# Kernel tuning notes

Measured on AMD Instinct MI355X. Metric: run time of the kernel, lower is better.

## Reference

```python
import jax, jax.numpy as jnp
import numpy as np


def setup_inputs() -> dict:
    key = jax.random.key(0)
    k1, k2, k3 = jax.random.split(key, 3)
    bs, seqlen, hidden = 2, 2048, 1024
    s, h = 4, 256  # sqrt_n_heads, head_size
    std = 0.02
    num_layers = 12
    hidden_states = jax.random.normal(k1, (bs, seqlen, hidden), dtype=jnp.float32)
    q_scale = 1.0 / np.sqrt(2.0 * num_layers * h)
    queries = jax.random.normal(k2, (s, h, h * s), dtype=jnp.float32) * std * q_scale
    combiners = jax.random.normal(k3, (s, h * s, h), dtype=jnp.float32) * (std * q_scale)
    return {"hidden_states": hidden_states, "queries": queries, "combiners": combiners}


def reference(hidden_states, queries, combiners):
    # queries: [s1, h, s*h], combiners: [s1, s*h, h]
    s, h, _ = queries.shape
    bs, S, E = hidden_states.shape
    x = hidden_states.reshape(bs, S, s, h)            # [b, t, s, h]
    qw = queries.reshape(s, h, s, h)                  # [s1, h_in, s2, h_out]
    # projected queries, already permuted to [s2, b, t, s1, f]
    Q = jnp.einsum('btae,aeqf->qbtaf', x, qw)
    # pre-attention scores: [s2, b, t, s1, u] (u = key position)  ~O(S^2)
    pre = jnp.einsum('qbtaf,buqf->qbtau', Q, x)
    # attention output, permuted to [s1, b, t, s2, g]
    attn = jnp.einsum('qbtau,buqg->abtqg', pre, x)
    attn = attn.reshape(s, bs, S, s * h)              # [s1, b, t, s2*h]
    out = jnp.einsum('abtk,akg->btag', attn, combiners)
    return out.reshape(bs, S, s * h)
```

## Files before the change

### kernel.cpp

```cpp
#include <hip/hip_runtime.h>
#include <hip/hip_bf16.h>


typedef unsigned short u16;
using short8  = __attribute__((ext_vector_type(8))) short;
using floatx4 = __attribute__((ext_vector_type(4))) float;

__device__ inline u16 f2bf(float f) {
    unsigned u = __float_as_uint(f);
    unsigned r = u + 0x7fffu + ((u >> 16) & 1u);
    return (u16)(r >> 16);
}

template <typename T>
__device__ inline void stage64(const T* __restrict__ src, long ld,
                               u16* __restrict__ dst, int tid) {
#pragma unroll
    for (int it = 0; it < 4; ++it) {
        const int flat = (it * 256 + tid) * 4;
        const int kl = flat & 63, rl = flat >> 6;
        ushort4 v;
        if (sizeof(T) == 4) {
            const float4 f = *(const float4*)&((const float*)src)[(long)rl * ld + kl];
            v.x = f2bf(f.x); v.y = f2bf(f.y); v.z = f2bf(f.z); v.w = f2bf(f.w);
        } else {
            v = *(const ushort4*)&((const u16*)src)[(long)rl * ld + kl];
        }
        const int chunk = ((kl >> 5) * 4 + (rl >> 4)) * 64 + ((kl >> 3) & 3) * 16 + (rl & 15);
        *(ushort4*)&dst[chunk * 8 + (kl & 7)] = v;
    }
}

__device__ inline void stage64_sum8(const float* __restrict__ s0, long ld,
                                    long partStride,
                                    u16* __restrict__ dst, int tid) {
#pragma unroll
    for (int it = 0; it < 4; ++it) {
        const int flat = (it * 256 + tid) * 4;
        const int kl = flat & 63, rl = flat >> 6;
        const long off = (long)rl * ld + kl;
        float4 acc = *(const float4*)&s0[off];
#pragma unroll
        for (int s = 1; s < 8; ++s) {
            const float4 f = *(const float4*)&s0[(long)s * partStride + off];
            acc.x += f.x; acc.y += f.y; acc.z += f.z; acc.w += f.w;
        }
        ushort4 v;
        v.x = f2bf(acc.x); v.y = f2bf(acc.y); v.z = f2bf(acc.z); v.w = f2bf(acc.w);
        const int chunk = ((kl >> 5) * 4 + (rl >> 4)) * 64 + ((kl >> 3) & 3) * 16 + (rl & 15);
        *(ushort4*)&dst[chunk * 8 + (kl & 7)] = v;
    }
}

__device__ inline void stage_km64(const float* __restrict__ src, long ld,
                                  u16* __restrict__ dst, int tid) {
#pragma unroll
    for (int it = 0; it < 4; ++it) {
        const int flat = (it * 256 + tid) * 4;
        const int m = flat & 63, k = flat >> 6;
        const float4 f = *(const float4*)&src[(long)k * ld + m];
        const int cb_ = ((k >> 5) * 4 + (m >> 4)) * 64 + ((k & 31) >> 3) * 16 + (m & 15);
        const int j = k & 7;
        dst[(cb_ + 0) * 8 + j] = f2bf(f.x);
        dst[(cb_ + 1) * 8 + j] = f2bf(f.y);
        dst[(cb_ + 2) * 8 + j] = f2bf(f.z);
        dst[(cb_ + 3) * 8 + j] = f2bf(f.w);
    }
}

template <typename TA, typename TB, typename TC,
          bool AKM, bool BKM, bool BSUM8, bool ATOMIC>
__device__ inline void gemm_tile(const TA* __restrict__ A, long lda,
                                 const TB* __restrict__ B, long ldb,
                                 long partStride,
                                 TC* __restrict__ C, long ldc,
                                 int m0, int n0) {
    __shared__ u16 As[16384];
    __shared__ u16 Bs[16384];
    const int tid = threadIdx.x, lane = tid & 63, w = tid >> 6;
    const int IA = (w & 1) * 2, JB = (w >> 1) * 2;
    floatx4 acc[2][2] = {};

#pragma unroll
    for (int kb = 0; kb < 4; ++kb) {
        if (AKM) stage_km64((const float*)A + (long)(kb * 64) * lda, lda, As + kb * 4096, tid);
        else     stage64(A + kb * 64, lda, As + kb * 4096, tid);
    }
#pragma unroll
    for (int kb = 0; kb < 4; ++kb) {
        if (BSUM8)    stage64_sum8((const float*)B + kb * 64, ldb, partStride, Bs + kb * 4096, tid);
        else if (BKM) stage_km64((const float*)B + (long)(kb * 64) * ldb, ldb, Bs + kb * 4096, tid);
        else          stage64(B + kb * 64, ldb, Bs + kb * 4096, tid);
    }
    __syncthreads();

#pragma unroll
    for (int kb = 0; kb < 4; ++kb)
#pragma unroll
        for (int s = 0; s < 2; ++s) {
            short8 af[2], bfr[2];
#pragma unroll
            for (int i = 0; i < 2; ++i)
                af[i] = *(const short8*)&As[kb * 4096 + ((s * 4 + IA + i) * 64 + lane) * 8];
#pragma unroll
            for (int j = 0; j < 2; ++j)
                bfr[j] = *(const short8*)&Bs[kb * 4096 + ((s * 4 + JB + j) * 64 + lane) * 8];
#pragma unroll
            for (int i = 0; i < 2; ++i)
#pragma unroll
                for (int j = 0; j < 2; ++j)
                    acc[i][j] = __builtin_amdgcn_mfma_f32_16x16x32_bf16(af[i], bfr[j], acc[i][j], 0, 0, 0);
        }

    const int rb = (lane >> 4) * 4, col = lane & 15;
#pragma unroll
    for (int i = 0; i < 2; ++i)
#pragma unroll
        for (int j = 0; j < 2; ++j)
#pragma unroll
            for (int r = 0; r < 4; ++r) {
                const int gm = m0 + (IA + i) * 16 + rb + r;
                const int gn = n0 + (JB + j) * 16 + col;
                TC* p = &C[(long)gm * ldc + gn];
                if (sizeof(TC) == 2) *(u16*)p = f2bf(acc[i][j][r]);
                else if (ATOMIC) atomicAdd((float*)p, acc[i][j][r]);
                else *(float*)p = acc[i][j][r];
            }
}

__device__ inline void stage_km128(const float* __restrict__ src, long ld,
                                   u16* __restrict__ dst, int tid) {
#pragma unroll
    for (int it = 0; it < 8; ++it) {
        const int flat = (it * 256 + tid) * 4;
        const int m = flat & 127, k = flat >> 7;
        const float4 f = *(const float4*)&src[(long)k * ld + m];
        const int cb_ = ((k >> 5) * 8 + (m >> 4)) * 64 + ((k & 31) >> 3) * 16 + (m & 15);
        const int j = k & 7;
        dst[(cb_ + 0) * 8 + j] = f2bf(f.x);
        dst[(cb_ + 1) * 8 + j] = f2bf(f.y);
        dst[(cb_ + 2) * 8 + j] = f2bf(f.z);
        dst[(cb_ + 3) * 8 + j] = f2bf(f.w);
    }
}

__global__ __launch_bounds__(256) void k_gram(const float* __restrict__ x,
                                              float* __restrict__ Gp,
                                              float* __restrict__ Wt) {
    __shared__ u16 As[16384];
    __shared__ u16 Bs[16384];
    const int tl = blockIdx.x, bq = blockIdx.y, split = blockIdx.z;
    const int tm = tl >> 1, tn = tl & 1;
    const int b = bq >> 2, q = bq & 3;
    const int tid = threadIdx.x, lane = tid & 63, w = tid >> 6;
    const int IA2 = (w & 1), JB2 = (w >> 1);

    {
        const int bl = tl + 4 * bq + 32 * split;
        float4 zero = {0.f, 0.f, 0.f, 0.f};
        float4* wz = (float4*)(Wt + (long)bl * 2048) + tid;
        wz[0] = zero; wz[256] = zero;
    }

    const float* base = x + (long)b * 2097152 + (long)split * 256 * 1024 + q * 256;
    const float* A = base + tm * 128;
    const float* B = base + tn * 128;
    floatx4 acc[4][4] = {};

#pragma unroll
    for (int burst = 0; burst < 2; ++burst) {
        if (burst) __syncthreads();
#pragma unroll
        for (int kb = 0; kb < 2; ++kb) {
            const long kk = burst * 128 + kb * 64;
            stage_km128(A + kk * 1024, 1024, As + kb * 8192, tid);
            stage_km128(B + kk * 1024, 1024, Bs + kb * 8192, tid);
        }
        __syncthreads();
#pragma unroll
        for (int kb = 0; kb < 2; ++kb)
#pragma unroll
            for (int s = 0; s < 2; ++s) {
                short8 af[4], bfr[4];
#pragma unroll
                for (int i = 0; i < 4; ++i)
                    af[i] = *(const short8*)&As[kb * 8192 + ((s * 8 + IA2 * 4 + i) * 64 + lane) * 8];
#pragma unroll
                for (int j = 0; j < 4; ++j)
                    bfr[j] = *(const short8*)&Bs[kb * 8192 + ((s * 8 + JB2 * 4 + j) * 64 + lane) * 8];
#pragma unroll
                for (int i = 0; i < 4; ++i)
#pragma unroll
                    for (int j = 0; j < 4; ++j)
                        acc[i][j] = __builtin_amdgcn_mfma_f32_16x16x32_bf16(af[i], bfr[j], acc[i][j], 0, 0, 0);
            }
    }

    float* C = Gp + (long)(split * 8 + bq) * 65536;
    const int rb = (lane >> 4) * 4, col = lane & 15;
#pragma unroll
    for (int i = 0; i < 4; ++i)
#pragma unroll
        for (int j = 0; j < 4; ++j)
#pragma unroll
            for (int r = 0; r < 4; ++r) {
                const int gm = tm * 128 + IA2 * 64 + i * 16 + rb + r;
                const int gn = tn * 128 + JB2 * 64 + j * 16 + col;
                C[(long)gm * 256 + gn] = acc[i][j][r];
            }
}

__global__ __launch_bounds__(256) void k_2a(const float* __restrict__ comb,
                                            const float* __restrict__ Gp,
                                            u16* __restrict__ Tt) {
    const int tile = blockIdx.x, i = blockIdx.y;
    const int tm = tile >> 2, tn = tile & 3;
    const int q = i & 3, ba = i >> 2, b = ba >> 2, a = ba & 3;
    gemm_tile<float, float, u16, true, false, true, false>(
        comb + (long)a * 262144 + (long)q * 256 * 256 + tm * 64, 256,
        Gp + (long)(b * 4 + q) * 65536 + (long)tn * 64 * 256, 256,
        (long)8 * 65536,
        Tt + (long)ba * 262144, 1024,
        tm * 64, q * 256 + tn * 64);
}

__global__ __launch_bounds__(256) void k_2b(const u16* __restrict__ Tt,
                                            const float* __restrict__ qw,
                                            float* __restrict__ Wt) {
    const int tile = blockIdx.x, ba = blockIdx.y, split = blockIdx.z;
    const int tm = tile >> 2, tn = tile & 3;
    const int a = ba & 3;
    gemm_tile<u16, float, float, false, false, false, true>(
        Tt + (long)ba * 262144 + (long)tm * 64 * 1024 + split * 256, 1024,
        qw + (long)a * 262144 + (long)tn * 64 * 1024 + split * 256, 1024, 0,
        Wt + (long)ba * 65536, 256,
        tm * 64, tn * 64);
}

__global__ __launch_bounds__(256) void k_3(const float* __restrict__ x,
                                           const float* __restrict__ Wt,
                                           float* __restrict__ out) {
    const int tl = blockIdx.x, ba = blockIdx.y;
    const int tm = tl >> 2, tn = tl & 3;
    const int b = ba >> 2, a = ba & 3;
    gemm_tile<float, float, float, false, false, false, false>(
        x + (long)b * 2097152 + (long)tm * 64 * 1024 + a * 256, 1024,
        Wt + (long)ba * 65536 + (long)tn * 64 * 256, 256, 0,
        out + (long)b * 2097152 + a * 256, 1024,
        tm * 64, tn * 64);
}

extern "C" void kernel_launch(void* const* d_in, const int* in_sizes, int n_in,
                              void* d_out, int out_size, void* d_ws, size_t ws_size,
                              hipStream_t stream) {
    const float* x    = (const float*)d_in[0];
    const float* qw   = (const float*)d_in[1];
    const float* comb = (const float*)d_in[2];
    float* out = (float*)d_out;

    char* ws = (char*)d_ws;
    float* Gp = (float*)(ws);
    float* Wt = (float*)(ws + (16u << 20));
    u16*   Tt = (u16*)  (ws + (18u << 20));

    k_gram<<<dim3(4, 8, 8),  256, 0, stream>>>(x, Gp, Wt);
    k_2a  <<<dim3(16, 32),   256, 0, stream>>>(comb, Gp, Tt);
    k_2b  <<<dim3(16, 8, 4), 256, 0, stream>>>(Tt, qw, Wt);
    k_3   <<<dim3(128, 8),   256, 0, stream>>>(x, Wt, out);
}
```

Before: 137.6 us.

## Pre-convert input to bf16 once and add separate split-K reduction kernel

Adds a kernel that converts hidden_states to bf16 once, so the Gram and final GEMM kernels read half-size bf16 data instead of converting fp32 at every staging. Adds a separate reduction kernel that sums the eight split-K Gram partials into one buffer, so k_2a no longer sums partials while loading its operands. This trades two extra launches and extra workspace traffic for less redundant conversion and less load work in the downstream GEMMs.

```diff
diff --git a/kernel.cpp b/kernel.cpp
--- a/kernel.cpp
+++ b/kernel.cpp
@@ -128,23 +128,46 @@
             }
 }
 
-__device__ inline void stage_km128(const float* __restrict__ src, long ld,
-                                   u16* __restrict__ dst, int tid) {
-#pragma unroll
-    for (int it = 0; it < 8; ++it) {
-        const int flat = (it * 256 + tid) * 4;
+__global__ __launch_bounds__(256) void k_cvt(const float* __restrict__ x,
+                                             u16* __restrict__ xbf) {
+    const long i = ((long)blockIdx.x * 256 + threadIdx.x) * 8;
+    const float4 a = *(const float4*)&x[i];
+    const float4 b = *(const float4*)&x[i + 4];
+    ushort4 lo, hi;
+    lo.x = f2bf(a.x); lo.y = f2bf(a.y); lo.z = f2bf(a.z); lo.w = f2bf(a.w);
+    hi.x = f2bf(b.x); hi.y = f2bf(b.y); hi.z = f2bf(b.z); hi.w = f2bf(b.w);
+    *(ushort4*)&xbf[i]     = lo;
+    *(ushort4*)&xbf[i + 4] = hi;
+}
+
+__global__ __launch_bounds__(256) void k_gred(const float* __restrict__ Gp,
+                                              float* __restrict__ Gs) {
+    const long i = ((long)blockIdx.x * 256 + threadIdx.x) * 4;
+    float4 acc = *(const float4*)&Gp[i];
+#pragma unroll
+    for (int s = 1; s < 8; ++s) {
+        const float4 f = *(const float4*)&Gp[(long)s * 524288 + i];
+        acc.x += f.x; acc.y += f.y; acc.z += f.z; acc.w += f.w;
+    }
+    *(float4*)&Gs[i] = acc;
+}
+
+__device__ inline void stage_km128_bf(const u16* __restrict__ src, long ld,
+                                      u16* __restrict__ dst, int tid) {
+#pragma unroll
+    for (int it = 0; it < 4; ++it) {
+        const int flat = (it * 256 + tid) * 8;
         const int m = flat & 127, k = flat >> 7;
-        const float4 f = *(const float4*)&src[(long)k * ld + m];
+        const short8 v = *(const short8*)&src[(long)k * ld + m];
         const int cb_ = ((k >> 5) * 8 + (m >> 4)) * 64 + ((k & 31) >> 3) * 16 + (m & 15);
         const int j = k & 7;
-        dst[(cb_ + 0) * 8 + j] = f2bf(f.x);
-        dst[(cb_ + 1) * 8 + j] = f2bf(f.y);
-        dst[(cb_ + 2) * 8 + j] = f2bf(f.z);
-        dst[(cb_ + 3) * 8 + j] = f2bf(f.w);
-    }
-}
-
-__global__ __launch_bounds__(256) void k_gram(const float* __restrict__ x,
+#pragma unroll
+        for (int e = 0; e < 8; ++e)
+            dst[(cb_ + e) * 8 + j] = (u16)v[e];
+    }
+}
+
+__global__ __launch_bounds__(256) void k_gram(const u16* __restrict__ xbf,
                                               float* __restrict__ Gp,
                                               float* __restrict__ Wt) {
     __shared__ u16 As[16384];
@@ -162,9 +185,9 @@
         wz[0] = zero; wz[256] = zero;
     }
 
-    const float* base = x + (long)b * 2097152 + (long)split * 256 * 1024 + q * 256;
-    const float* A = base + tm * 128;
-    const float* B = base + tn * 128;
+    const u16* base = xbf + (long)b * 2097152 + (long)split * 256 * 1024 + q * 256;
+    const u16* A = base + tm * 128;
+    const u16* B = base + tn * 128;
     floatx4 acc[4][4] = {};
 
 #pragma unroll
@@ -173,8 +196,8 @@
 #pragma unroll
         for (int kb = 0; kb < 2; ++kb) {
             const long kk = burst * 128 + kb * 64;
-            stage_km128(A + kk * 1024, 1024, As + kb * 8192, tid);
-            stage_km128(B + kk * 1024, 1024, Bs + kb * 8192, tid);
+            stage_km128_bf(A + kk * 1024, 1024, As + kb * 8192, tid);
+            stage_km128_bf(B + kk * 1024, 1024, Bs + kb * 8192, tid);
         }
         __syncthreads();
 #pragma unroll
@@ -211,15 +234,15 @@
 }
 
 __global__ __launch_bounds__(256) void k_2a(const float* __restrict__ comb,
-                                            const float* __restrict__ Gp,
+                                            const float* __restrict__ Gs,
                                             u16* __restrict__ Tt) {
     const int tile = blockIdx.x, i = blockIdx.y;
     const int tm = tile >> 2, tn = tile & 3;
     const int q = i & 3, ba = i >> 2, b = ba >> 2, a = ba & 3;
-    gemm_tile<float, float, u16, true, false, true, false>(
+    gemm_tile<float, float, u16, true, false, false, false>(
         comb + (long)a * 262144 + (long)q * 256 * 256 + tm * 64, 256,
-        Gp + (long)(b * 4 + q) * 65536 + (long)tn * 64 * 256, 256,
-        (long)8 * 65536,
+        Gs + (long)(b * 4 + q) * 65536 + (long)tn * 64 * 256, 256,
+        0,
         Tt + (long)ba * 262144, 1024,
         tm * 64, q * 256 + tn * 64);
 }
@@ -237,14 +260,14 @@
         tm * 64, tn * 64);
 }
 
-__global__ __launch_bounds__(256) void k_3(const float* __restrict__ x,
+__global__ __launch_bounds__(256) void k_3(const u16* __restrict__ xbf,
                                            const float* __restrict__ Wt,
                                            float* __restrict__ out) {
     const int tl = blockIdx.x, ba = blockIdx.y;
     const int tm = tl >> 2, tn = tl & 3;
     const int b = ba >> 2, a = ba & 3;
-    gemm_tile<float, float, float, false, false, false, false>(
-        x + (long)b * 2097152 + (long)tm * 64 * 1024 + a * 256, 1024,
+    gemm_tile<u16, float, float, false, false, false, false>(
+        xbf + (long)b * 2097152 + (long)tm * 64 * 1024 + a * 256, 1024,
         Wt + (long)ba * 65536 + (long)tn * 64 * 256, 256, 0,
         out + (long)b * 2097152 + a * 256, 1024,
         tm * 64, tn * 64);
@@ -262,9 +285,13 @@
     float* Gp = (float*)(ws);
     float* Wt = (float*)(ws + (16u << 20));
     u16*   Tt = (u16*)  (ws + (18u << 20));
-
-    k_gram<<<dim3(4, 8, 8),  256, 0, stream>>>(x, Gp, Wt);
-    k_2a  <<<dim3(16, 32),   256, 0, stream>>>(comb, Gp, Tt);
+    float* Gs = (float*)(ws + (22u << 20));
+    u16*   xbf= (u16*)  (ws + (24u << 20));
+
+    k_cvt <<<dim3(2048),     256, 0, stream>>>(x, xbf);
+    k_gram<<<dim3(4, 8, 8),  256, 0, stream>>>(xbf, Gp, Wt);
+    k_gred<<<dim3(512),      256, 0, stream>>>(Gp, Gs);
+    k_2a  <<<dim3(16, 32),   256, 0, stream>>>(comb, Gs, Tt);
     k_2b  <<<dim3(16, 8, 4), 256, 0, stream>>>(Tt, qw, Wt);
-    k_3   <<<dim3(128, 8),   256, 0, stream>>>(x, Wt, out);
-}
+    k_3   <<<dim3(128, 8),   256, 0, stream>>>(xbf, Wt, out);
+}
```

Result: faster. 133.7 us (-2.8%).

## Pre-convert weights to bf16 in gram kernel, drop split-K atomics, store Wt bf16

Applied to the files above, without the earlier changes.

The gram kernel gains extra blocks that convert the query weights to bf16 and write a transposed bf16 copy of the combiners, so later GEMMs can use vectorized 16-byte bf16 staging instead of strided fp32 transposing stores. k_2b now loops over the full K inside one block instead of using split-K with atomicAdd, which removes the atomics and the zeroing of Wt. Wt is stored as bf16, which halves what k_3 reads. In exchange k_2b launches four times fewer blocks, and rounding Wt to bf16 adds precision loss.

```diff
diff --git a/kernel.cpp b/kernel.cpp
--- a/kernel.cpp
+++ b/kernel.cpp
@@ -1,5 +1,4 @@
 #include <hip/hip_runtime.h>
-#include <hip/hip_bf16.h>
 
 
 typedef unsigned short u16;
@@ -12,20 +11,27 @@
     return (u16)(r >> 16);
 }
 
-template <typename T>
-__device__ inline void stage64(const T* __restrict__ src, long ld,
-                               u16* __restrict__ dst, int tid) {
+__device__ inline void stage64_bf(const u16* __restrict__ src, long ld,
+                                  u16* __restrict__ dst, int tid) {
+#pragma unroll
+    for (int it = 0; it < 2; ++it) {
+        const int flat = (it * 256 + tid) * 8;
+        const int kl = flat & 63, rl = flat >> 6;
+        const short8 v = *(const short8*)&src[(long)rl * ld + kl];
+        const int chunk = ((kl >> 5) * 4 + (rl >> 4)) * 64 + ((kl >> 3) & 3) * 16 + (rl & 15);
+        *(short8*)&dst[chunk * 8] = v;
+    }
+}
+
+__device__ inline void stage64_f32(const float* __restrict__ src, long ld,
+                                   u16* __restrict__ dst, int tid) {
 #pragma unroll
     for (int it = 0; it < 4; ++it) {
         const int flat = (it * 256 + tid) * 4;
         const int kl = flat & 63, rl = flat >> 6;
+        const float4 f = *(const float4*)&src[(long)rl * ld + kl];
         ushort4 v;
-        if (sizeof(T) == 4) {
-            const float4 f = *(const float4*)&((const float*)src)[(long)rl * ld + kl];
-            v.x = f2bf(f.x); v.y = f2bf(f.y); v.z = f2bf(f.z); v.w = f2bf(f.w);
-        } else {
-            v = *(const ushort4*)&((const u16*)src)[(long)rl * ld + kl];
-        }
+        v.x = f2bf(f.x); v.y = f2bf(f.y); v.z = f2bf(f.z); v.w = f2bf(f.w);
         const int chunk = ((kl >> 5) * 4 + (rl >> 4)) * 64 + ((kl >> 3) & 3) * 16 + (rl & 15);
         *(ushort4*)&dst[chunk * 8 + (kl & 7)] = v;
     }
@@ -50,82 +56,6 @@
         const int chunk = ((kl >> 5) * 4 + (rl >> 4)) * 64 + ((kl >> 3) & 3) * 16 + (rl & 15);
         *(ushort4*)&dst[chunk * 8 + (kl & 7)] = v;
     }
-}
-
-__device__ inline void stage_km64(const float* __restrict__ src, long ld,
-                                  u16* __restrict__ dst, int tid) {
-#pragma unroll
-    for (int it = 0; it < 4; ++it) {
-        const int flat = (it * 256 + tid) * 4;
-        const int m = flat & 63, k = flat >> 6;
-        const float4 f = *(const float4*)&src[(long)k * ld + m];
-        const int cb_ = ((k >> 5) * 4 + (m >> 4)) * 64 + ((k & 31) >> 3) * 16 + (m & 15);
-        const int j = k & 7;
-        dst[(cb_ + 0) * 8 + j] = f2bf(f.x);
-        dst[(cb_ + 1) * 8 + j] = f2bf(f.y);
-        dst[(cb_ + 2) * 8 + j] = f2bf(f.z);
-        dst[(cb_ + 3) * 8 + j] = f2bf(f.w);
-    }
-}
-
-template <typename TA, typename TB, typename TC,
-          bool AKM, bool BKM, bool BSUM8, bool ATOMIC>
-__device__ inline void gemm_tile(const TA* __restrict__ A, long lda,
-                                 const TB* __restrict__ B, long ldb,
-                                 long partStride,
-                                 TC* __restrict__ C, long ldc,
-                                 int m0, int n0) {
-    __shared__ u16 As[16384];
-    __shared__ u16 Bs[16384];
-    const int tid = threadIdx.x, lane = tid & 63, w = tid >> 6;
-    const int IA = (w & 1) * 2, JB = (w >> 1) * 2;
-    floatx4 acc[2][2] = {};
-
-#pragma unroll
-    for (int kb = 0; kb < 4; ++kb) {
-        if (AKM) stage_km64((const float*)A + (long)(kb * 64) * lda, lda, As + kb * 4096, tid);
-        else     stage64(A + kb * 64, lda, As + kb * 4096, tid);
-    }
-#pragma unroll
-    for (int kb = 0; kb < 4; ++kb) {
-        if (BSUM8)    stage64_sum8((const float*)B + kb * 64, ldb, partStride, Bs + kb * 4096, tid);
-        else if (BKM) stage_km64((const float*)B + (long)(kb * 64) * ldb, ldb, Bs + kb * 4096, tid);
-        else          stage64(B + kb * 64, ldb, Bs + kb * 4096, tid);
-    }
-    __syncthreads();
-
-#pragma unroll
-    for (int kb = 0; kb < 4; ++kb)
-#pragma unroll
-        for (int s = 0; s < 2; ++s) {
-            short8 af[2], bfr[2];
-#pragma unroll
-            for (int i = 0; i < 2; ++i)
-                af[i] = *(const short8*)&As[kb * 4096 + ((s * 4 + IA + i) * 64 + lane) * 8];
-#pragma unroll
-            for (int j = 0; j < 2; ++j)
-                bfr[j] = *(const short8*)&Bs[kb * 4096 + ((s * 4 + JB + j) * 64 + lane) * 8];
-#pragma unroll
-            for (int i = 0; i < 2; ++i)
-#pragma unroll
-                for (int j = 0; j < 2; ++j)
-                    acc[i][j] = __builtin_amdgcn_mfma_f32_16x16x32_bf16(af[i], bfr[j], acc[i][j], 0, 0, 0);
-        }
-
-    const int rb = (lane >> 4) * 4, col = lane & 15;
-#pragma unroll
-    for (int i = 0; i < 2; ++i)
-#pragma unroll
-        for (int j = 0; j < 2; ++j)
-#pragma unroll
-            for (int r = 0; r < 4; ++r) {
-                const int gm = m0 + (IA + i) * 16 + rb + r;
-                const int gn = n0 + (JB + j) * 16 + col;
-                TC* p = &C[(long)gm * ldc + gn];
-                if (sizeof(TC) == 2) *(u16*)p = f2bf(acc[i][j][r]);
-                else if (ATOMIC) atomicAdd((float*)p, acc[i][j][r]);
-                else *(float*)p = acc[i][j][r];
-            }
 }
 
 __device__ inline void stage_km128(const float* __restrict__ src, long ld,
@@ -144,108 +74,205 @@
     }
 }
 
-__global__ __launch_bounds__(256) void k_gram(const float* __restrict__ x,
-                                              float* __restrict__ Gp,
-                                              float* __restrict__ Wt) {
+template <int AM, int BM, typename TC, int KR>
+__device__ inline void gemm_tile(const void* __restrict__ Av, long lda,
+                                 const void* __restrict__ Bv, long ldb,
+                                 long partStride,
+                                 TC* __restrict__ C, long ldc,
+                                 int m0, int n0) {
     __shared__ u16 As[16384];
     __shared__ u16 Bs[16384];
-    const int tl = blockIdx.x, bq = blockIdx.y, split = blockIdx.z;
-    const int tm = tl >> 1, tn = tl & 1;
-    const int b = bq >> 2, q = bq & 3;
     const int tid = threadIdx.x, lane = tid & 63, w = tid >> 6;
-    const int IA2 = (w & 1), JB2 = (w >> 1);
-
-    {
-        const int bl = tl + 4 * bq + 32 * split;
-        float4 zero = {0.f, 0.f, 0.f, 0.f};
-        float4* wz = (float4*)(Wt + (long)bl * 2048) + tid;
-        wz[0] = zero; wz[256] = zero;
-    }
-
-    const float* base = x + (long)b * 2097152 + (long)split * 256 * 1024 + q * 256;
-    const float* A = base + tm * 128;
-    const float* B = base + tn * 128;
-    floatx4 acc[4][4] = {};
-
-#pragma unroll
-    for (int burst = 0; burst < 2; ++burst) {
-        if (burst) __syncthreads();
-#pragma unroll
-        for (int kb = 0; kb < 2; ++kb) {
-            const long kk = burst * 128 + kb * 64;
-            stage_km128(A + kk * 1024, 1024, As + kb * 8192, tid);
-            stage_km128(B + kk * 1024, 1024, Bs + kb * 8192, tid);
+    const int IA = (w & 1) * 2, JB = (w >> 1) * 2;
+    floatx4 acc[2][2] = {};
+
+#pragma unroll
+    for (int r = 0; r < KR; ++r) {
+        if (r) __syncthreads();
+#pragma unroll
+        for (int kb = 0; kb < 4; ++kb) {
+            if (AM == 0) stage64_bf ((const u16*)Av   + r * 256 + kb * 64, lda, As + kb * 4096, tid);
+            else         stage64_f32((const float*)Av + r * 256 + kb * 64, lda, As + kb * 4096, tid);
+            if (BM == 0)      stage64_bf  ((const u16*)Bv   + r * 256 + kb * 64, ldb, Bs + kb * 4096, tid);
+            else if (BM == 1) stage64_f32 ((const float*)Bv + r * 256 + kb * 64, ldb, Bs + kb * 4096, tid);
+            else              stage64_sum8((const float*)Bv + kb * 64, ldb, partStride, Bs + kb * 4096, tid);
         }
         __syncthreads();
-#pragma unroll
-        for (int kb = 0; kb < 2; ++kb)
+
+#pragma unroll
+        for (int kb = 0; kb < 4; ++kb)
 #pragma unroll
             for (int s = 0; s < 2; ++s) {
-                short8 af[4], bfr[4];
-#pragma unroll
-                for (int i = 0; i < 4; ++i)
-                    af[i] = *(const short8*)&As[kb * 8192 + ((s * 8 + IA2 * 4 + i) * 64 + lane) * 8];
-#pragma unroll
-                for (int j = 0; j < 4; ++j)
-                    bfr[j] = *(const short8*)&Bs[kb * 8192 + ((s * 8 + JB2 * 4 + j) * 64 + lane) * 8];
-#pragma unroll
-                for (int i = 0; i < 4; ++i)
+                short8 af[2], bfr[2];
+#pragma unroll
+                for (int i = 0; i < 2; ++i)
+                    af[i] = *(const short8*)&As[kb * 4096 + ((s * 4 + IA + i) * 64 + lane) * 8];
+#pragma unroll
+                for (int j = 0; j < 2; ++j)
+                    bfr[j] = *(const short8*)&Bs[kb * 4096 + ((s * 4 + JB + j) * 64 + lane) * 8];
+#pragma unroll
+                for (int i = 0; i < 2; ++i)
+#pragma unroll
+                    for (int j = 0; j < 2; ++j)
+                        acc[i][j] = __builtin_amdgcn_mfma_f32_16x16x32_bf16(af[i], bfr[j], acc[i][j], 0, 0, 0);
+            }
+    }
+
+    const int rb = (lane >> 4) * 4, col = lane & 15;
+#pragma unroll
+    for (int i = 0; i < 2; ++i)
+#pragma unroll
+        for (int j = 0; j < 2; ++j)
+#pragma unroll
+            for (int r = 0; r < 4; ++r) {
+                const int gm = m0 + (IA + i) * 16 + rb + r;
+                const int gn = n0 + (JB + j) * 16 + col;
+                TC* p = &C[(long)gm * ldc + gn];
+                if (sizeof(TC) == 2) *(u16*)p = f2bf(acc[i][j][r]);
+                else                 *(float*)p = acc[i][j][r];
+            }
+}
+
+__global__ __launch_bounds__(256) void k_1(const float* __restrict__ x,
+                                           const float* __restrict__ qw,
+                                           const float* __restrict__ comb,
+                                           float* __restrict__ Gp,
+                                           u16* __restrict__ qwbf,
+                                           u16* __restrict__ combt) {
+    __shared__ u16 As[16384];
+    __shared__ u16 Bs[16384];
+    const int bid = blockIdx.x, tid = threadIdx.x;
+
+    if (bid < 256) {
+        const int tl = bid & 3, bq = (bid >> 2) & 7, split = bid >> 5;
+        const int tm = tl >> 1, tn = tl & 1;
+        const int b = bq >> 2, q = bq & 3;
+        const int lane = tid & 63, w = tid >> 6;
+        const int IA2 = (w & 1), JB2 = (w >> 1);
+
+        const float* base = x + (long)b * 2097152 + (long)split * 262144 + q * 256;
+        const float* A = base + tm * 128;
+        const float* B = base + tn * 128;
+        floatx4 acc[4][4] = {};
+
+#pragma unroll
+        for (int burst = 0; burst < 2; ++burst) {
+            if (burst) __syncthreads();
+#pragma unroll
+            for (int kb = 0; kb < 2; ++kb) {
+                const long kk = burst * 128 + kb * 64;
+                stage_km128(A + kk * 1024, 1024, As + kb * 8192, tid);
+                stage_km128(B + kk * 1024, 1024, Bs + kb * 8192, tid);
+            }
+            __syncthreads();
+#pragma unroll
+            for (int kb = 0; kb < 2; ++kb)
+#pragma unroll
+                for (int s = 0; s < 2; ++s) {
+                    short8 af[4], bfr[4];
+#pragma unroll
+                    for (int i = 0; i < 4; ++i)
+                        af[i] = *(const short8*)&As[kb * 8192 + ((s * 8 + IA2 * 4 + i) * 64 + lane) * 8];
 #pragma unroll
                     for (int j = 0; j < 4; ++j)
-                        acc[i][j] = __builtin_amdgcn_mfma_f32_16x16x32_bf16(af[i], bfr[j], acc[i][j], 0, 0, 0);
-            }
-    }
-
-    float* C = Gp + (long)(split * 8 + bq) * 65536;
-    const int rb = (lane >> 4) * 4, col = lane & 15;
-#pragma unroll
-    for (int i = 0; i < 4; ++i)
-#pragma unroll
-        for (int j = 0; j < 4; ++j)
-#pragma unroll
-            for (int r = 0; r < 4; ++r) {
-                const int gm = tm * 128 + IA2 * 64 + i * 16 + rb + r;
-                const int gn = tn * 128 + JB2 * 64 + j * 16 + col;
-                C[(long)gm * 256 + gn] = acc[i][j][r];
-            }
-}
-
-__global__ __launch_bounds__(256) void k_2a(const float* __restrict__ comb,
+                        bfr[j] = *(const short8*)&Bs[kb * 8192 + ((s * 8 + JB2 * 4 + j) * 64 + lane) * 8];
+#pragma unroll
+                    for (int i = 0; i < 4; ++i)
+#pragma unroll
+                        for (int j = 0; j < 4; ++j)
+                            acc[i][j] = __builtin_amdgcn_mfma_f32_16x16x32_bf16(af[i], bfr[j], acc[i][j], 0, 0, 0);
+                }
+        }
+
+        float* C = Gp + (long)(split * 8 + bq) * 65536;
+        const int rb = (lane >> 4) * 4, col = lane & 15;
+#pragma unroll
+        for (int i = 0; i < 4; ++i)
+#pragma unroll
+            for (int j = 0; j < 4; ++j)
+#pragma unroll
+                for (int r = 0; r < 4; ++r) {
+                    const int gm = tm * 128 + IA2 * 64 + i * 16 + rb + r;
+                    const int gn = tn * 128 + JB2 * 64 + j * 16 + col;
+                    C[(long)gm * 256 + gn] = acc[i][j][r];
+                }
+    } else {
+        for (int u = bid - 256; u < 768; u += 64) {
+            if (u < 512) {
+                const long i = ((long)u * 256 + tid) * 8;
+                const float4 a = *(const float4*)&qw[i];
+                const float4 b = *(const float4*)&qw[i + 4];
+                ushort4 lo, hi;
+                lo.x = f2bf(a.x); lo.y = f2bf(a.y); lo.z = f2bf(a.z); lo.w = f2bf(a.w);
+                hi.x = f2bf(b.x); hi.y = f2bf(b.y); hi.z = f2bf(b.z); hi.w = f2bf(b.w);
+                *(ushort4*)&qwbf[i]     = lo;
+                *(ushort4*)&qwbf[i + 4] = hi;
+            } else {
+                u16 (*T)[66] = (u16(*)[66])As;
+                const int t = u - 512;
+                const int a = t >> 6;
+                const int qh0 = ((t >> 2) & 15) * 64, g0 = (t & 3) * 64;
+                const float* src = comb + (long)a * 262144;
+                u16* dst = combt + (long)a * 262144;
+                __syncthreads();
+#pragma unroll
+                for (int it = 0; it < 4; ++it) {
+                    const int flat = (it * 256 + tid) * 4;
+                    const int r = flat >> 6, c = flat & 63;
+                    const float4 f = *(const float4*)&src[(long)(qh0 + r) * 256 + g0 + c];
+                    T[r][c]     = f2bf(f.x); T[r][c + 1] = f2bf(f.y);
+                    T[r][c + 2] = f2bf(f.z); T[r][c + 3] = f2bf(f.w);
+                }
+                __syncthreads();
+#pragma unroll
+                for (int it = 0; it < 4; ++it) {
+                    const int flat = (it * 256 + tid) * 4;
+                    const int r = flat >> 6, c = flat & 63;
+                    ushort4 v;
+                    v.x = T[c][r]; v.y = T[c + 1][r]; v.z = T[c + 2][r]; v.w = T[c + 3][r];
+                    *(ushort4*)&dst[(long)(g0 + r) * 1024 + qh0 + c] = v;
+                }
+            }
+        }
+    }
+}
+
+__global__ __launch_bounds__(256) void k_2a(const u16* __restrict__ combt,
                                             const float* __restrict__ Gp,
                                             u16* __restrict__ Tt) {
     const int tile = blockIdx.x, i = blockIdx.y;
     const int tm = tile >> 2, tn = tile & 3;
     const int q = i & 3, ba = i >> 2, b = ba >> 2, a = ba & 3;
-    gemm_tile<float, float, u16, true, false, true, false>(
-        comb + (long)a * 262144 + (long)q * 256 * 256 + tm * 64, 256,
-        Gp + (long)(b * 4 + q) * 65536 + (long)tn * 64 * 256, 256,
-        (long)8 * 65536,
+    gemm_tile<0, 2, u16, 1>(
+        combt + (long)a * 262144 + (long)tm * 65536 + q * 256, 1024,
+        Gp + (long)(b * 4 + q) * 65536 + (long)tn * 16384, 256,
+        524288,
         Tt + (long)ba * 262144, 1024,
         tm * 64, q * 256 + tn * 64);
 }
 
 __global__ __launch_bounds__(256) void k_2b(const u16* __restrict__ Tt,
-                                            const float* __restrict__ qw,
-                                            float* __restrict__ Wt) {
-    const int tile = blockIdx.x, ba = blockIdx.y, split = blockIdx.z;
+                                            const u16* __restrict__ qwbf,
+                                            u16* __restrict__ Wt) {
+    const int tile = blockIdx.x, ba = blockIdx.y;
     const int tm = tile >> 2, tn = tile & 3;
     const int a = ba & 3;
-    gemm_tile<u16, float, float, false, false, false, true>(
-        Tt + (long)ba * 262144 + (long)tm * 64 * 1024 + split * 256, 1024,
-        qw + (long)a * 262144 + (long)tn * 64 * 1024 + split * 256, 1024, 0,
+    gemm_tile<0, 0, u16, 4>(
+        Tt + (long)ba * 262144 + (long)tm * 65536, 1024,
+        qwbf + (long)a * 262144 + (long)tn * 65536, 1024, 0,
         Wt + (long)ba * 65536, 256,
         tm * 64, tn * 64);
 }
 
 __global__ __launch_bounds__(256) void k_3(const float* __restrict__ x,
-                                           const float* __restrict__ Wt,
+                                           const u16* __restrict__ Wt,
                                            float* __restrict__ out) {
     const int tl = blockIdx.x, ba = blockIdx.y;
     const int tm = tl >> 2, tn = tl & 3;
     const int b = ba >> 2, a = ba & 3;
-    gemm_tile<float, float, float, false, false, false, false>(
-        x + (long)b * 2097152 + (long)tm * 64 * 1024 + a * 256, 1024,
-        Wt + (long)ba * 65536 + (long)tn * 64 * 256, 256, 0,
+    gemm_tile<1, 0, float, 1>(
+        x + (long)b * 2097152 + (long)tm * 65536 + a * 256, 1024,
+        Wt + (long)ba * 65536 + (long)tn * 16384, 256, 0,
         out + (long)b * 2097152 + a * 256, 1024,
         tm * 64, tn * 64);
 }
@@ -259,12 +286,14 @@
     float* out = (float*)d_out;
 
     char* ws = (char*)d_ws;
-    float* Gp = (float*)(ws);
-    float* Wt = (float*)(ws + (16u << 20));
-    u16*   Tt = (u16*)  (ws + (18u << 20));
-
-    k_gram<<<dim3(4, 8, 8),  256, 0, stream>>>(x, Gp, Wt);
-    k_2a  <<<dim3(16, 32),   256, 0, stream>>>(comb, Gp, Tt);
-    k_2b  <<<dim3(16, 8, 4), 256, 0, stream>>>(Tt, qw, Wt);
-    k_3   <<<dim3(128, 8),   256, 0, stream>>>(x, Wt, out);
-}
+    float* Gp   = (float*)(ws);
+    u16*   Tt   = (u16*)  (ws + (16u << 20));
+    u16*   qwbf = (u16*)  (ws + (20u << 20));
+    u16*   combt= (u16*)  (ws + (22u << 20));
+    u16*   Wtbf = (u16*)  (ws + (24u << 20));
+
+    k_1 <<<dim3(320),    256, 0, stream>>>(x, qw, comb, Gp, qwbf, combt);
+    k_2a<<<dim3(16, 32), 256, 0, stream>>>(combt, Gp, Tt);
+    k_2b<<<dim3(16, 8),  256, 0, stream>>>(Tt, qwbf, Wtbf);
+    k_3 <<<dim3(128, 8), 256, 0, stream>>>(x, Wtbf, out);
+}
```

Result: faster. 134.2 us (-2.5%).
